# Optimization experiments

Hardware: AMD Instinct MI355X
Metric: run time of the kernel (lower is better)

The kernel has to match this reference:

```python
import jax, jax.numpy as jnp
import numpy as np

N_ATOMS, N_UND, N_DIR, N_ANG, N_STRUCT = 8192, 65536, 131072, 262144, 128
FEA, NRAD, NANGB, NCONV = 64, 9, 9, 4

FLOAT_NAMES = ["bond_bases_ag", "bond_bases_bg", "angle_bases", "atom_emb", "Wb", "Wa",
               "Wbw_ag", "Wbw_bg",
               "ac_cw1", "ac_cb1", "ac_cw2", "ac_cb2", "ac_gw1", "ac_gb1", "ac_gw2", "ac_gb2", "ac_out",
               "bc_cw1", "bc_cb1", "bc_cw2", "bc_cb2", "bc_gw1", "bc_gb1", "bc_gw2", "bc_gb2", "bc_out",
               "an_cw", "an_cb", "an_gw", "an_gb",
               "ro_w1", "ro_b1", "ro_w2", "ro_b2", "ro_w3", "ro_b3"]
INT_NAMES = ["atomic_numbers", "atom_graph", "directed2undirected",
             "bond_graph_atoms", "bond_graph_bonds", "atom_owners"]


def _silu(x):
    return x * jax.nn.sigmoid(x)


def _gmlp(x, cw1, cb1, cw2, cb2, gw1, gb1, gw2, gb2):
    # GatedMLP (norm=None): silu(MLP_core(x)) * sigmoid(MLP_gate(x)), each MLP = Lin-silu-Lin
    core = _silu(_silu(x @ cw1 + cb1) @ cw2 + cb2)
    gate = jax.nn.sigmoid(_silu(x @ gw1 + gb1) @ gw2 + gb2)
    return core * gate


def _forward(F, I):
    seg = jax.ops.segment_sum
    atom = F["atom_emb"][I["atomic_numbers"]]            # [N, 64]
    bond = F["bond_bases_ag"] @ F["Wb"]                  # [U, 64]
    angle = F["angle_bases"] @ F["Wa"]                   # [A, 64]
    bw_ag = F["bond_bases_ag"] @ F["Wbw_ag"]             # [U, 64]
    bw_bg = F["bond_bases_bg"] @ F["Wbw_bg"]             # [U, 64]
    ag0, ag1 = I["atom_graph"][:, 0], I["atom_graph"][:, 1]
    d2u = I["directed2undirected"]
    bgi, bgj = I["bond_graph_bonds"][:, 0], I["bond_graph_bonds"][:, 1]
    bga = I["bond_graph_atoms"]

    def atom_conv(i, atom, bond):
        msg = jnp.concatenate([atom[ag0], bond[d2u], atom[ag1]], axis=1)   # [E, 192]
        msg = _gmlp(msg, F["ac_cw1"][i], F["ac_cb1"][i], F["ac_cw2"][i], F["ac_cb2"][i],
                    F["ac_gw1"][i], F["ac_gb1"][i], F["ac_gw2"][i], F["ac_gb2"][i])
        msg = msg * bw_ag[d2u]
        # scatter-add to center atoms, linear mlp_out (no bias), resnet
        return atom + seg(msg, ag0, num_segments=N_ATOMS) @ F["ac_out"][i]

    for i in range(NCONV - 1):
        atom = atom_conv(i, atom, bond)
        # BondConv over bond graph (angles)
        tot = jnp.concatenate([bond[bgi], bond[bgj], angle, atom[bga]], axis=1)  # [A, 256]
        upd = _gmlp(tot, F["bc_cw1"][i], F["bc_cb1"][i], F["bc_cw2"][i], F["bc_cb2"][i],
                    F["bc_gw1"][i], F["bc_gb1"][i], F["bc_gw2"][i], F["bc_gb2"][i])
        upd = upd * bw_bg[bgi]
        bond = bond + seg(upd, bgi, num_segments=N_UND) @ F["bc_out"][i]
        # AngleUpdate (hidden_dim=0 -> single linear in each gated branch), resnet
        tot2 = jnp.concatenate([bond[bgi], bond[bgj], angle, atom[bga]], axis=1)
        angle = angle + _silu(tot2 @ F["an_cw"][i] + F["an_cb"][i]) * \
            jax.nn.sigmoid(tot2 @ F["an_gw"][i] + F["an_gb"][i])
    atom = atom_conv(NCONV - 1, atom, bond)

    # mlp_first readout: per-atom energy MLP then average pooling per structure
    e = _silu(atom @ F["ro_w1"] + F["ro_b1"])
    e = _silu(e @ F["ro_w2"] + F["ro_b2"])
    e = (e @ F["ro_w3"] + F["ro_b3"])[:, 0]              # [N]
    owners = I["atom_owners"]
    esum = seg(e, owners, num_segments=N_STRUCT)
    cnt = seg(jnp.ones_like(e), owners, num_segments=N_STRUCT)
    return esum / jnp.maximum(cnt, 1.0)                  # [N_STRUCT] energy/atom


def setup_inputs() -> dict:
    key = jax.random.key(0)
    ks = iter(jax.random.split(key, 64))

    def nrm(shape, fan_in):
        return jax.random.normal(next(ks), shape, dtype=jnp.float32) / np.float32(np.sqrt(fan_in))

    z = lambda *s: jnp.zeros(s, dtype=jnp.float32)
    inp = {}
    inp["atomic_numbers"] = jax.random.randint(next(ks), (N_ATOMS,), 0, 94, dtype=jnp.int32)
    inp["bond_bases_ag"] = jax.random.uniform(next(ks), (N_UND, NRAD), dtype=jnp.float32)
    inp["bond_bases_bg"] = jax.random.uniform(next(ks), (N_UND, NRAD), dtype=jnp.float32)
    inp["angle_bases"] = jax.random.uniform(next(ks), (N_ANG, NANGB), dtype=jnp.float32)
    inp["atom_graph"] = jax.random.randint(next(ks), (N_DIR, 2), 0, N_ATOMS, dtype=jnp.int32)
    inp["directed2undirected"] = jax.random.randint(next(ks), (N_DIR,), 0, N_UND, dtype=jnp.int32)
    inp["bond_graph_atoms"] = jax.random.randint(next(ks), (N_ANG,), 0, N_ATOMS, dtype=jnp.int32)
    inp["bond_graph_bonds"] = jax.random.randint(next(ks), (N_ANG, 2), 0, N_UND, dtype=jnp.int32)
    inp["atom_owners"] = jnp.sort(jax.random.randint(next(ks), (N_ATOMS,), 0, N_STRUCT, dtype=jnp.int32))
    inp["atom_emb"] = nrm((95, FEA), 1.0)
    inp["Wb"] = nrm((NRAD, FEA), NRAD)
    inp["Wa"] = nrm((NANGB, FEA), NANGB)
    inp["Wbw_ag"] = nrm((NRAD, FEA), NRAD)
    inp["Wbw_bg"] = nrm((NRAD, FEA), NRAD)
    d_a, d_b = 3 * FEA, 4 * FEA
    nb = NCONV - 1
    inp["ac_cw1"] = nrm((NCONV, d_a, FEA), d_a); inp["ac_cb1"] = z(NCONV, FEA)
    inp["ac_cw2"] = nrm((NCONV, FEA, FEA), FEA); inp["ac_cb2"] = z(NCONV, FEA)
    inp["ac_gw1"] = nrm((NCONV, d_a, FEA), d_a); inp["ac_gb1"] = z(NCONV, FEA)
    inp["ac_gw2"] = nrm((NCONV, FEA, FEA), FEA); inp["ac_gb2"] = z(NCONV, FEA)
    inp["ac_out"] = nrm((NCONV, FEA, FEA), FEA)
    inp["bc_cw1"] = nrm((nb, d_b, FEA), d_b); inp["bc_cb1"] = z(nb, FEA)
    inp["bc_cw2"] = nrm((nb, FEA, FEA), FEA); inp["bc_cb2"] = z(nb, FEA)
    inp["bc_gw1"] = nrm((nb, d_b, FEA), d_b); inp["bc_gb1"] = z(nb, FEA)
    inp["bc_gw2"] = nrm((nb, FEA, FEA), FEA); inp["bc_gb2"] = z(nb, FEA)
    inp["bc_out"] = nrm((nb, FEA, FEA), FEA)
    inp["an_cw"] = nrm((nb, d_b, FEA), d_b); inp["an_cb"] = z(nb, FEA)
    inp["an_gw"] = nrm((nb, d_b, FEA), d_b); inp["an_gb"] = z(nb, FEA)
    inp["ro_w1"] = nrm((FEA, FEA), FEA); inp["ro_b1"] = z(FEA)
    inp["ro_w2"] = nrm((FEA, FEA), FEA); inp["ro_b2"] = z(FEA)
    inp["ro_w3"] = nrm((FEA, 1), FEA); inp["ro_b3"] = z(1)
    return inp


def reference(atomic_numbers, bond_bases_ag, bond_bases_bg, angle_bases, atom_graph,
              directed2undirected, bond_graph_atoms, bond_graph_bonds, atom_owners,
              atom_emb, Wb, Wa, Wbw_ag, Wbw_bg,
              ac_cw1, ac_cb1, ac_cw2, ac_cb2, ac_gw1, ac_gb1, ac_gw2, ac_gb2, ac_out,
              bc_cw1, bc_cb1, bc_cw2, bc_cb2, bc_gw1, bc_gb1, bc_gw2, bc_gb2, bc_out,
              an_cw, an_cb, an_gw, an_gb,
              ro_w1, ro_b1, ro_w2, ro_b2, ro_w3, ro_b3):
    loc = locals()
    F = {k: loc[k] for k in FLOAT_NAMES}
    I = {k: loc[k] for k in INT_NAMES}
    return _forward(F, I)
```

## Files before the change

### kernel.cpp

```cpp
#include <hip/hip_runtime.h>
#include <hip/hip_bf16.h>

typedef float f32x4 __attribute__((ext_vector_type(4)));
typedef short s16x8 __attribute__((ext_vector_type(8)));
typedef unsigned int u32x4 __attribute__((ext_vector_type(4)));

#define DEV static __device__ __forceinline__

DEV unsigned short f2bf(float x){
    unsigned u = __builtin_bit_cast(unsigned, x);
    u += 0x7FFFu + ((u >> 16) & 1u);
    return (unsigned short)(u >> 16);
}
DEV float bf2f(unsigned short h){
    unsigned u = ((unsigned)h) << 16;
    return __builtin_bit_cast(float, u);
}
DEV float sigm_(float x){ return __builtin_amdgcn_rcpf(1.0f + __expf(-x)); }
DEV float silu_(float x){ return x * sigm_(x); }

__global__ __launch_bounds__(256) void k_transconv(const float* __restrict__ src,
                                                   unsigned short* __restrict__ dst,
                                                   int K, int total){
    int gid = blockIdx.x * 256 + threadIdx.x;
    if (gid >= total) return;
    int kn  = K * 64;
    int b   = gid / kn;
    int rem = gid - b * kn;
    int k   = rem >> 6, n = rem & 63;
    dst[b * kn + n * K + k] = f2bf(src[gid]);
}

__global__ __launch_bounds__(256) void k_embed(const float* __restrict__ emb,
                                               const int* __restrict__ z,
                                               unsigned short* __restrict__ out){
    int gid = blockIdx.x * 256 + threadIdx.x;
    int n = gid >> 6, f = gid & 63;
    out[gid] = f2bf(emb[z[n] * 64 + f]);
}

__global__ __launch_bounds__(256) void k_smallmm(const float* __restrict__ bases,
                                                 const float* __restrict__ W,
                                                 unsigned short* __restrict__ out){
    int gid = blockIdx.x * 256 + threadIdx.x;
    int r = gid >> 6, f = gid & 63;
    const float* b = bases + r * 9;
    float acc = 0.f;
    #pragma unroll
    for (int k = 0; k < 9; ++k) acc += b[k] * W[k * 64 + f];
    out[gid] = f2bf(acc);
}

__global__ void k_count(const int* __restrict__ dst, int stride, int n, int* __restrict__ cnt){
    int i = blockIdx.x * 256 + threadIdx.x;
    if (i < n) atomicAdd(&cnt[dst[(size_t)i * stride]], 1);
}

__global__ __launch_bounds__(256) void k_bsum(const int* __restrict__ cnt,
                                              int* __restrict__ bsum){
    int i = blockIdx.x * 256 + threadIdx.x;
    int v = cnt[i];
    #pragma unroll
    for (int off = 32; off > 0; off >>= 1) v += __shfl_down(v, off);
    __shared__ int ws[4];
    if ((threadIdx.x & 63) == 0) ws[threadIdx.x >> 6] = v;
    __syncthreads();
    if (threadIdx.x == 0) bsum[blockIdx.x] = ws[0] + ws[1] + ws[2] + ws[3];
}

__global__ __launch_bounds__(256) void k_bscan(const int* __restrict__ bsum,
                                               int* __restrict__ bbase, int nb,
                                               int* __restrict__ total_out){
    __shared__ int sh[256];
    int t = threadIdx.x;
    int v = (t < nb) ? bsum[t] : 0;
    sh[t] = v;
    __syncthreads();
    for (int d = 1; d < 256; d <<= 1){
        int u = (t >= d) ? sh[t - d] : 0;
        __syncthreads();
        sh[t] += u;
        __syncthreads();
    }
    if (t < nb) bbase[t] = sh[t] - v;
    if (t == nb - 1) *total_out = sh[t];
}

__global__ __launch_bounds__(256) void k_offs(const int* __restrict__ cnt,
                                              const int* __restrict__ bbase,
                                              int* __restrict__ offs){
    __shared__ int sh[256];
    int t = threadIdx.x;
    int i = blockIdx.x * 256 + t;
    int v = cnt[i];
    sh[t] = v;
    __syncthreads();
    for (int d = 1; d < 256; d <<= 1){
        int u = (t >= d) ? sh[t - d] : 0;
        __syncthreads();
        sh[t] += u;
        __syncthreads();
    }
    offs[i] = bbase[blockIdx.x] + sh[t] - v;
}

__global__ void k_fill(const int* __restrict__ dst, int stride, int n,
                       const int* __restrict__ offs, int* __restrict__ cur,
                       int* __restrict__ idx){
    int i = blockIdx.x * 256 + threadIdx.x;
    if (i < n){
        int d = dst[(size_t)i * stride];
        int p = offs[d] + atomicAdd(&cur[d], 1);
        idx[p] = i;
    }
}

__global__ __launch_bounds__(256) void k_reduce(const unsigned short* __restrict__ upd,
                                                const int* __restrict__ offs,
                                                const int* __restrict__ idx,
                                                unsigned short* __restrict__ act, int nRows){
    int gid = blockIdx.x * 256 + threadIdx.x;
    int row = gid >> 3;
    if (row >= nRows) return;
    int c8 = (gid & 7) * 8;
    int o = offs[row], e = offs[row + 1];
    float acc[8] = {};
    for (int j = o; j < e; ++j){
        s16x8 v = *(const s16x8*)&upd[(size_t)idx[j] * 64 + c8];
        #pragma unroll
        for (int q = 0; q < 8; ++q) acc[q] += bf2f((unsigned short)v[q]);
    }
    s16x8 a = *(s16x8*)&act[(size_t)row * 64 + c8];
    #pragma unroll
    for (int q = 0; q < 8; ++q) a[q] = (short)f2bf(bf2f((unsigned short)a[q]) + acc[q]);
    *(s16x8*)&act[(size_t)row * 64 + c8] = a;
}

#define MFMA16(a,b,c) __builtin_amdgcn_mfma_f32_16x16x32_bf16(a,b,c,0,0,0)

__global__ __launch_bounds__(256, 4) void k_atom_conv(
    const unsigned short* __restrict__ atomBf, const unsigned short* __restrict__ bondBf,
    const unsigned short* __restrict__ bwagBf,
    const int* __restrict__ agraph, const int* __restrict__ d2u,
    const unsigned short* __restrict__ w1cT, const unsigned short* __restrict__ w1gT,
    const unsigned short* __restrict__ w2cT, const unsigned short* __restrict__ w2gT,
    const unsigned short* __restrict__ woT,
    const float* __restrict__ cb1, const float* __restrict__ cb2,
    const float* __restrict__ gb1, const float* __restrict__ gb2,
    unsigned short* __restrict__ upd)
{
    __shared__ unsigned short lds[14208];
    __shared__ int ldsIdx[64];
    unsigned short* ldsA  = lds;
    unsigned short* ldsHC = lds;
    unsigned short* ldsHG = lds + 4736;
    unsigned short* ldsV  = lds + 9472;
    const int tid = threadIdx.x;
    const int r0  = blockIdx.x * 64;

    {
        const int srow = tid >> 2, q = tid & 3;
        int e = r0 + srow;
        if (q < 3){
            const unsigned short* src;
            if (q == 0)      src = atomBf + (size_t)agraph[2 * e] * 64;
            else if (q == 1){ int u = d2u[e]; ldsIdx[srow] = u; src = bondBf + (size_t)u * 64; }
            else             src = atomBf + (size_t)agraph[2 * e + 1] * 64;
            #pragma unroll
            for (int j = 0; j < 8; ++j)
                *(u32x4*)&ldsA[srow * 200 + q * 64 + j * 8] = *(const u32x4*)(src + j * 8);
        }
    }
    __syncthreads();

    const int lane = tid & 63;
    const int r16  = lane & 15;
    const int grp  = lane >> 4;
    const int col  = (tid >> 6) * 16 + r16;

    unsigned short bwv[16];
    #pragma unroll
    for (int mt = 0; mt < 4; ++mt)
        #pragma unroll
        for (int j = 0; j < 4; ++j)
            bwv[mt * 4 + j] = bwagBf[(size_t)ldsIdx[mt * 16 + grp * 4 + j] * 64 + col];

    f32x4 aC[4] = {}, aG[4] = {};
    #pragma unroll
    for (int kt = 0; kt < 6; ++kt){
        s16x8 bc = *(const s16x8*)&w1cT[col * 192 + kt * 32 + grp * 8];
        s16x8 bg = *(const s16x8*)&w1gT[col * 192 + kt * 32 + grp * 8];
        #pragma unroll
        for (int mt = 0; mt < 4; ++mt){
            s16x8 a = *(const s16x8*)&ldsA[(mt * 16 + r16) * 200 + kt * 32 + grp * 8];
            aC[mt] = MFMA16(a, bc, aC[mt]);
            aG[mt] = MFMA16(a, bg, aG[mt]);
        }
    }
    __syncthreads();

    const float bC1 = cb1[col], bG1 = gb1[col];
    #pragma unroll
    for (int mt = 0; mt < 4; ++mt){
        #pragma unroll
        for (int j = 0; j < 4; ++j){
            int row = mt * 16 + grp * 4 + j;
            ldsHC[row * 74 + col] = f2bf(silu_(aC[mt][j] + bC1));
            ldsHG[row * 74 + col] = f2bf(silu_(aG[mt][j] + bG1));
        }
    }
    __syncthreads();

    f32x4 oC[4] = {}, oG[4] = {};
    #pragma unroll
    for (int kt = 0; kt < 2; ++kt){
        s16x8 bc = *(const s16x8*)&w2cT[col * 64 + kt * 32 + grp * 8];
        s16x8 bg = *(const s16x8*)&w2gT[col * 64 + kt * 32 + grp * 8];
        #pragma unroll
        for (int mt = 0; mt < 4; ++mt){
            s16x8 hc = *(const s16x8*)&ldsHC[(mt * 16 + r16) * 74 + kt * 32 + grp * 8];
            s16x8 hg = *(const s16x8*)&ldsHG[(mt * 16 + r16) * 74 + kt * 32 + grp * 8];
            oC[mt] = MFMA16(hc, bc, oC[mt]);
            oG[mt] = MFMA16(hg, bg, oG[mt]);
        }
    }
    const float bC2 = cb2[col], bG2 = gb2[col];
    #pragma unroll
    for (int mt = 0; mt < 4; ++mt){
        #pragma unroll
        for (int j = 0; j < 4; ++j){
            int row = mt * 16 + grp * 4 + j;
            float v = silu_(oC[mt][j] + bC2) * sigm_(oG[mt][j] + bG2);
            v *= bf2f(bwv[mt * 4 + j]);
            ldsV[row * 74 + col] = f2bf(v);
        }
    }
    __syncthreads();

    f32x4 oD[4] = {};
    #pragma unroll
    for (int kt = 0; kt < 2; ++kt){
        s16x8 bo = *(const s16x8*)&woT[col * 64 + kt * 32 + grp * 8];
        #pragma unroll
        for (int mt = 0; mt < 4; ++mt){
            s16x8 a = *(const s16x8*)&ldsV[(mt * 16 + r16) * 74 + kt * 32 + grp * 8];
            oD[mt] = MFMA16(a, bo, oD[mt]);
        }
    }
    #pragma unroll
    for (int mt = 0; mt < 4; ++mt){
        #pragma unroll
        for (int j = 0; j < 4; ++j){
            int row = mt * 16 + grp * 4 + j;
            upd[(size_t)(r0 + row) * 64 + col] = f2bf(oD[mt][j]);
        }
    }
}

__global__ __launch_bounds__(256, 4) void k_bond_conv(
    const unsigned short* __restrict__ atomBf, const unsigned short* __restrict__ bondBf,
    const unsigned short* __restrict__ angleBf, const unsigned short* __restrict__ bwbgBf,
    const int* __restrict__ bga, const int* __restrict__ bgb,
    const unsigned short* __restrict__ w1cT, const unsigned short* __restrict__ w1gT,
    const unsigned short* __restrict__ w2cT, const unsigned short* __restrict__ w2gT,
    const unsigned short* __restrict__ woT,
    const float* __restrict__ cb1, const float* __restrict__ cb2,
    const float* __restrict__ gb1, const float* __restrict__ gb2,
    unsigned short* __restrict__ upd)
{
    __shared__ unsigned short lds[16896];
    __shared__ int ldsIdx[64];
    unsigned short* ldsA  = lds;
    unsigned short* ldsHC = lds;
    unsigned short* ldsHG = lds + 4736;
    unsigned short* ldsV  = lds + 9472;
    const int tid = threadIdx.x;
    const int r0  = blockIdx.x * 64;

    {
        const int srow = tid >> 2, q = tid & 3;
        int a = r0 + srow;
        const unsigned short* src;
        if (q == 0){ int2 bb = *(const int2*)&bgb[2 * a]; ldsIdx[srow] = bb.x;
                     src = bondBf + (size_t)bb.x * 64; }
        else if (q == 1){ src = bondBf  + (size_t)bgb[2 * a + 1] * 64; }
        else if (q == 2){ src = angleBf + (size_t)a * 64; }
        else            { src = atomBf  + (size_t)bga[a] * 64; }
        #pragma unroll
        for (int j = 0; j < 8; ++j)
            *(u32x4*)&ldsA[srow * 264 + q * 64 + j * 8] = *(const u32x4*)(src + j * 8);
    }
    __syncthreads();

    const int lane = tid & 63;
    const int r16  = lane & 15;
    const int grp  = lane >> 4;
    const int col  = (tid >> 6) * 16 + r16;

    unsigned short bwv[16];
    #pragma unroll
    for (int mt = 0; mt < 4; ++mt)
        #pragma unroll
        for (int j = 0; j < 4; ++j)
            bwv[mt * 4 + j] = bwbgBf[(size_t)ldsIdx[mt * 16 + grp * 4 + j] * 64 + col];

    f32x4 aC[4] = {}, aG[4] = {};
    #pragma unroll
    for (int kt = 0; kt < 8; ++kt){
        s16x8 bc = *(const s16x8*)&w1cT[col * 256 + kt * 32 + grp * 8];
        s16x8 bg = *(const s16x8*)&w1gT[col * 256 + kt * 32 + grp * 8];
        #pragma unroll
        for (int mt = 0; mt < 4; ++mt){
            s16x8 a = *(const s16x8*)&ldsA[(mt * 16 + r16) * 264 + kt * 32 + grp * 8];
            aC[mt] = MFMA16(a, bc, aC[mt]);
            aG[mt] = MFMA16(a, bg, aG[mt]);
        }
    }
    __syncthreads();

    const float bC1 = cb1[col], bG1 = gb1[col];
    #pragma unroll
    for (int mt = 0; mt < 4; ++mt){
        #pragma unroll
        for (int j = 0; j < 4; ++j){
            int row = mt * 16 + grp * 4 + j;
            ldsHC[row * 74 + col] = f2bf(silu_(aC[mt][j] + bC1));
            ldsHG[row * 74 + col] = f2bf(silu_(aG[mt][j] + bG1));
        }
    }
    __syncthreads();

    f32x4 oC[4] = {}, oG[4] = {};
    #pragma unroll
    for (int kt = 0; kt < 2; ++kt){
        s16x8 bc = *(const s16x8*)&w2cT[col * 64 + kt * 32 + grp * 8];
        s16x8 bg = *(const s16x8*)&w2gT[col * 64 + kt * 32 + grp * 8];
        #pragma unroll
        for (int mt = 0; mt < 4; ++mt){
            s16x8 hc = *(const s16x8*)&ldsHC[(mt * 16 + r16) * 74 + kt * 32 + grp * 8];
            s16x8 hg = *(const s16x8*)&ldsHG[(mt * 16 + r16) * 74 + kt * 32 + grp * 8];
            oC[mt] = MFMA16(hc, bc, oC[mt]);
            oG[mt] = MFMA16(hg, bg, oG[mt]);
        }
    }
    const float bC2 = cb2[col], bG2 = gb2[col];
    #pragma unroll
    for (int mt = 0; mt < 4; ++mt){
        #pragma unroll
        for (int j = 0; j < 4; ++j){
            int row = mt * 16 + grp * 4 + j;
            float v = silu_(oC[mt][j] + bC2) * sigm_(oG[mt][j] + bG2);
            v *= bf2f(bwv[mt * 4 + j]);
            ldsV[row * 74 + col] = f2bf(v);
        }
    }
    __syncthreads();

    f32x4 oD[4] = {};
    #pragma unroll
    for (int kt = 0; kt < 2; ++kt){
        s16x8 bo = *(const s16x8*)&woT[col * 64 + kt * 32 + grp * 8];
        #pragma unroll
        for (int mt = 0; mt < 4; ++mt){
            s16x8 a = *(const s16x8*)&ldsV[(mt * 16 + r16) * 74 + kt * 32 + grp * 8];
            oD[mt] = MFMA16(a, bo, oD[mt]);
        }
    }
    #pragma unroll
    for (int mt = 0; mt < 4; ++mt){
        #pragma unroll
        for (int j = 0; j < 4; ++j){
            int row = mt * 16 + grp * 4 + j;
            upd[(size_t)(r0 + row) * 64 + col] = f2bf(oD[mt][j]);
        }
    }
}

__global__ __launch_bounds__(256, 4) void k_angle(
    const unsigned short* __restrict__ atomBf, const unsigned short* __restrict__ bondBf,
    unsigned short* __restrict__ angleBf,
    const int* __restrict__ bga, const int* __restrict__ bgb,
    const unsigned short* __restrict__ wcT, const unsigned short* __restrict__ wgT,
    const float* __restrict__ cb, const float* __restrict__ gb)
{
    __shared__ unsigned short ldsA[64 * 264];
    const int tid = threadIdx.x;
    const int r0  = blockIdx.x * 64;

    {
        const int srow = tid >> 2, q = tid & 3;
        int a = r0 + srow;
        const unsigned short* src;
        if (q == 0)      src = bondBf  + (size_t)bgb[2 * a] * 64;
        else if (q == 1) src = bondBf  + (size_t)bgb[2 * a + 1] * 64;
        else if (q == 2) src = angleBf + (size_t)a * 64;
        else             src = atomBf  + (size_t)bga[a] * 64;
        #pragma unroll
        for (int j = 0; j < 8; ++j)
            *(u32x4*)&ldsA[srow * 264 + q * 64 + j * 8] = *(const u32x4*)(src + j * 8);
    }
    __syncthreads();

    const int lane = tid & 63;
    const int r16  = lane & 15;
    const int grp  = lane >> 4;
    const int col  = (tid >> 6) * 16 + r16;

    f32x4 aC[4] = {}, aG[4] = {};
    #pragma unroll
    for (int kt = 0; kt < 8; ++kt){
        s16x8 bc = *(const s16x8*)&wcT[col * 256 + kt * 32 + grp * 8];
        s16x8 bg = *(const s16x8*)&wgT[col * 256 + kt * 32 + grp * 8];
        #pragma unroll
        for (int mt = 0; mt < 4; ++mt){
            s16x8 a = *(const s16x8*)&ldsA[(mt * 16 + r16) * 264 + kt * 32 + grp * 8];
            aC[mt] = MFMA16(a, bc, aC[mt]);
            aG[mt] = MFMA16(a, bg, aG[mt]);
        }
    }
    const float bC = cb[col], bG = gb[col];
    #pragma unroll
    for (int mt = 0; mt < 4; ++mt){
        #pragma unroll
        for (int j = 0; j < 4; ++j){
            int row = mt * 16 + grp * 4 + j;
            int a = r0 + row;
            float oldv = bf2f(ldsA[row * 264 + 128 + col]);
            float v = silu_(aC[mt][j] + bC) * sigm_(aG[mt][j] + bG);
            angleBf[(size_t)a * 64 + col] = f2bf(oldv + v);
        }
    }
}

__global__ __launch_bounds__(256) void k_readout(
    const unsigned short* __restrict__ atomBf, const int* __restrict__ owners,
    const float* __restrict__ w1, const float* __restrict__ b1,
    const float* __restrict__ w2, const float* __restrict__ b2,
    const float* __restrict__ w3, const float* __restrict__ b3,
    float* __restrict__ esum, float* __restrict__ cnt)
{
    int gid  = blockIdx.x * 256 + threadIdx.x;
    int n    = gid >> 6;
    int lane = threadIdx.x & 63;
    float a = bf2f(atomBf[n * 64 + lane]);
    float acc = b1[lane];
    #pragma unroll
    for (int k = 0; k < 64; ++k) acc += __shfl(a, k) * w1[k * 64 + lane];
    float h = silu_(acc);
    acc = b2[lane];
    #pragma unroll
    for (int k = 0; k < 64; ++k) acc += __shfl(h, k) * w2[k * 64 + lane];
    h = silu_(acc);
    float p = h * w3[lane];
    #pragma unroll
    for (int off = 32; off > 0; off >>= 1) p += __shfl_xor(p, off);
    if (lane == 0){
        atomicAdd(&esum[owners[n]], p + b3[0]);
        atomicAdd(&cnt[owners[n]], 1.0f);
    }
}

__global__ void k_final(const float* __restrict__ esum, const float* __restrict__ cnt,
                        float* __restrict__ out){
    int i = threadIdx.x;
    if (i < 128) out[i] = esum[i] / fmaxf(cnt[i], 1.0f);
}

extern "C" void kernel_launch(void* const* d_in, const int* in_sizes, int n_in,
                              void* d_out, int out_size, void* d_ws, size_t ws_size,
                              hipStream_t stream)
{
    (void)in_sizes; (void)n_in; (void)out_size; (void)ws_size;
    const int N_ATOMS = 8192, N_UND = 65536, N_DIR = 131072, N_ANG = 262144;

    const int*   atomic_numbers = (const int*)  d_in[0];
    const float* bb_ag  = (const float*)d_in[1];
    const float* bb_bg  = (const float*)d_in[2];
    const float* ang_b  = (const float*)d_in[3];
    const int*   agraph = (const int*)  d_in[4];
    const int*   d2u    = (const int*)  d_in[5];
    const int*   bga    = (const int*)  d_in[6];
    const int*   bgb    = (const int*)  d_in[7];
    const int*   owners = (const int*)  d_in[8];
    const float* emb    = (const float*)d_in[9];
    const float* Wb     = (const float*)d_in[10];
    const float* Wa     = (const float*)d_in[11];
    const float* Wbwag  = (const float*)d_in[12];
    const float* Wbwbg  = (const float*)d_in[13];
    const float* ac_cw1 = (const float*)d_in[14];
    const float* ac_cb1 = (const float*)d_in[15];
    const float* ac_cw2 = (const float*)d_in[16];
    const float* ac_cb2 = (const float*)d_in[17];
    const float* ac_gw1 = (const float*)d_in[18];
    const float* ac_gb1 = (const float*)d_in[19];
    const float* ac_gw2 = (const float*)d_in[20];
    const float* ac_gb2 = (const float*)d_in[21];
    const float* ac_out = (const float*)d_in[22];
    const float* bc_cw1 = (const float*)d_in[23];
    const float* bc_cb1 = (const float*)d_in[24];
    const float* bc_cw2 = (const float*)d_in[25];
    const float* bc_cb2 = (const float*)d_in[26];
    const float* bc_gw1 = (const float*)d_in[27];
    const float* bc_gb1 = (const float*)d_in[28];
    const float* bc_gw2 = (const float*)d_in[29];
    const float* bc_gb2 = (const float*)d_in[30];
    const float* bc_out = (const float*)d_in[31];
    const float* an_cw  = (const float*)d_in[32];
    const float* an_cb  = (const float*)d_in[33];
    const float* an_gw  = (const float*)d_in[34];
    const float* an_gb  = (const float*)d_in[35];
    const float* ro_w1  = (const float*)d_in[36];
    const float* ro_b1  = (const float*)d_in[37];
    const float* ro_w2  = (const float*)d_in[38];
    const float* ro_b2  = (const float*)d_in[39];
    const float* ro_w3  = (const float*)d_in[40];
    const float* ro_b3  = (const float*)d_in[41];

    char* ws = (char*)d_ws;
    size_t off = 0;
    auto alloc = [&](size_t bytes) -> void* {
        void* p = ws + off;
        off = (off + bytes + 255) & ~(size_t)255;
        return p;
    };
    unsigned short* atomBf  = (unsigned short*)alloc((size_t)N_ATOMS * 64 * 2);
    unsigned short* bondBf  = (unsigned short*)alloc((size_t)N_UND   * 64 * 2);
    unsigned short* angleBf = (unsigned short*)alloc((size_t)N_ANG   * 64 * 2);
    unsigned short* bwagBf  = (unsigned short*)alloc((size_t)N_UND   * 64 * 2);
    unsigned short* bwbgBf  = (unsigned short*)alloc((size_t)N_UND   * 64 * 2);
    unsigned short* updBuf  = (unsigned short*)alloc((size_t)N_ANG   * 64 * 2);
    float* esum   = (float*)alloc(128 * 4);
    float* cnt    = (float*)alloc(128 * 4);
    int* offsA = (int*)alloc((N_ATOMS + 1) * 4);
    int* curA  = (int*)alloc(N_ATOMS * 4);
    int* idxA  = (int*)alloc((size_t)N_DIR * 4);
    int* offsB = (int*)alloc((N_UND + 1) * 4);
    int* curB  = (int*)alloc(N_UND * 4);
    int* idxB  = (int*)alloc((size_t)N_ANG * 4);
    int* bsum  = (int*)alloc(256 * 4);
    int* bbase = (int*)alloc(256 * 4);
    unsigned short* acw1cT = (unsigned short*)alloc((size_t)4 * 64 * 192 * 2);
    unsigned short* acw1gT = (unsigned short*)alloc((size_t)4 * 64 * 192 * 2);
    unsigned short* acw2cT = (unsigned short*)alloc((size_t)4 * 64 * 64 * 2);
    unsigned short* acw2gT = (unsigned short*)alloc((size_t)4 * 64 * 64 * 2);
    unsigned short* acoT   = (unsigned short*)alloc((size_t)4 * 64 * 64 * 2);
    unsigned short* bcw1cT = (unsigned short*)alloc((size_t)3 * 64 * 256 * 2);
    unsigned short* bcw1gT = (unsigned short*)alloc((size_t)3 * 64 * 256 * 2);
    unsigned short* bcw2cT = (unsigned short*)alloc((size_t)3 * 64 * 64 * 2);
    unsigned short* bcw2gT = (unsigned short*)alloc((size_t)3 * 64 * 64 * 2);
    unsigned short* bcoT   = (unsigned short*)alloc((size_t)3 * 64 * 64 * 2);
    unsigned short* anwcT  = (unsigned short*)alloc((size_t)3 * 64 * 256 * 2);
    unsigned short* anwgT  = (unsigned short*)alloc((size_t)3 * 64 * 256 * 2);

    auto tc = [&](const float* src, unsigned short* dst, int B, int K){
        int total = B * K * 64;
        k_transconv<<<(total + 255) / 256, 256, 0, stream>>>(src, dst, K, total);
    };
    tc(ac_cw1, acw1cT, 4, 192);  tc(ac_gw1, acw1gT, 4, 192);
    tc(ac_cw2, acw2cT, 4, 64);   tc(ac_gw2, acw2gT, 4, 64);
    tc(ac_out, acoT,   4, 64);
    tc(bc_cw1, bcw1cT, 3, 256);  tc(bc_gw1, bcw1gT, 3, 256);
    tc(bc_cw2, bcw2cT, 3, 64);   tc(bc_gw2, bcw2gT, 3, 64);
    tc(bc_out, bcoT,   3, 64);
    tc(an_cw,  anwcT,  3, 256);  tc(an_gw,  anwgT,  3, 256);

    k_embed<<<N_ATOMS * 64 / 256, 256, 0, stream>>>(emb, atomic_numbers, atomBf);
    k_smallmm<<<N_UND * 64 / 256, 256, 0, stream>>>(bb_ag, Wb,    bondBf);
    k_smallmm<<<N_ANG * 64 / 256, 256, 0, stream>>>(ang_b, Wa,    angleBf);
    k_smallmm<<<N_UND * 64 / 256, 256, 0, stream>>>(bb_ag, Wbwag, bwagBf);
    k_smallmm<<<N_UND * 64 / 256, 256, 0, stream>>>(bb_bg, Wbwbg, bwbgBf);

    hipMemsetAsync(curA, 0, N_ATOMS * 4, stream);
    k_count<<<(N_DIR + 255) / 256, 256, 0, stream>>>(agraph, 2, N_DIR, curA);
    k_bsum <<<N_ATOMS / 256, 256, 0, stream>>>(curA, bsum);
    k_bscan<<<1, 256, 0, stream>>>(bsum, bbase, N_ATOMS / 256, offsA + N_ATOMS);
    k_offs <<<N_ATOMS / 256, 256, 0, stream>>>(curA, bbase, offsA);
    hipMemsetAsync(curA, 0, N_ATOMS * 4, stream);
    k_fill<<<(N_DIR + 255) / 256, 256, 0, stream>>>(agraph, 2, N_DIR, offsA, curA, idxA);

    hipMemsetAsync(curB, 0, N_UND * 4, stream);
    k_count<<<(N_ANG + 255) / 256, 256, 0, stream>>>(bgb, 2, N_ANG, curB);
    k_bsum <<<N_UND / 256, 256, 0, stream>>>(curB, bsum);
    k_bscan<<<1, 256, 0, stream>>>(bsum, bbase, N_UND / 256, offsB + N_UND);
    k_offs <<<N_UND / 256, 256, 0, stream>>>(curB, bbase, offsB);
    hipMemsetAsync(curB, 0, N_UND * 4, stream);
    k_fill<<<(N_ANG + 255) / 256, 256, 0, stream>>>(bgb, 2, N_ANG, offsB, curB, idxB);

    for (int i = 0; i < 4; ++i){
        k_atom_conv<<<N_DIR / 64, 256, 0, stream>>>(
            atomBf, bondBf, bwagBf, agraph, d2u,
            acw1cT + (size_t)i * 64 * 192, acw1gT + (size_t)i * 64 * 192,
            acw2cT + (size_t)i * 64 * 64,  acw2gT + (size_t)i * 64 * 64,
            acoT   + (size_t)i * 64 * 64,
            ac_cb1 + i * 64, ac_cb2 + i * 64, ac_gb1 + i * 64, ac_gb2 + i * 64, updBuf);
        k_reduce<<<N_ATOMS * 8 / 256, 256, 0, stream>>>(updBuf, offsA, idxA, atomBf, N_ATOMS);
        if (i == 3) break;
        k_bond_conv<<<N_ANG / 64, 256, 0, stream>>>(
            atomBf, bondBf, angleBf, bwbgBf, bga, bgb,
            bcw1cT + (size_t)i * 64 * 256, bcw1gT + (size_t)i * 64 * 256,
            bcw2cT + (size_t)i * 64 * 64,  bcw2gT + (size_t)i * 64 * 64,
            bcoT   + (size_t)i * 64 * 64,
            bc_cb1 + i * 64, bc_cb2 + i * 64, bc_gb1 + i * 64, bc_gb2 + i * 64, updBuf);
        k_reduce<<<N_UND * 8 / 256, 256, 0, stream>>>(updBuf, offsB, idxB, bondBf, N_UND);
        k_angle<<<N_ANG / 64, 256, 0, stream>>>(
            atomBf, bondBf, angleBf, bga, bgb,
            anwcT + (size_t)i * 64 * 256, anwgT + (size_t)i * 64 * 256,
            an_cb + i * 64, an_gb + i * 64);
    }

    hipMemsetAsync(esum, 0, 128 * 4, stream);
    hipMemsetAsync(cnt,  0, 128 * 4, stream);
    k_readout<<<N_ATOMS * 64 / 256, 256, 0, stream>>>(
        atomBf, owners, ro_w1, ro_b1, ro_w2, ro_b2, ro_w3, ro_b3, esum, cnt);
    k_final<<<1, 128, 0, stream>>>(esum, cnt, (float*)d_out);
}
```

Before: 913.2 us.

## Process edges in destination-sorted order so segment reduce reads contiguous rows

The atom, bond and angle conv kernels now visit edges and angles through the CSR permutation (idxA/idxB). They write each update row at its sorted position, so k_reduce sums a contiguous range instead of gathering rows through idx. The gather phase is rebuilt as two stages: first resolve source indices into LDS, then issue cooperative 16-byte row loads. The atom conv also stages the bw_ag rows in LDS instead of doing scattered per-element loads. This trades the reduce's indirect reads for one extra indirection in the conv kernels, plus angle writes that are now scattered.

```diff
diff --git a/kernel.cpp b/kernel.cpp
--- a/kernel.cpp
+++ b/kernel.cpp
@@ -117,7 +117,6 @@
 
 __global__ __launch_bounds__(256) void k_reduce(const unsigned short* __restrict__ upd,
                                                 const int* __restrict__ offs,
-                                                const int* __restrict__ idx,
                                                 unsigned short* __restrict__ act, int nRows){
     int gid = blockIdx.x * 256 + threadIdx.x;
     int row = gid >> 3;
@@ -126,7 +125,7 @@
     int o = offs[row], e = offs[row + 1];
     float acc[8] = {};
     for (int j = o; j < e; ++j){
-        s16x8 v = *(const s16x8*)&upd[(size_t)idx[j] * 64 + c8];
+        s16x8 v = *(const s16x8*)&upd[(size_t)j * 64 + c8];
         #pragma unroll
         for (int q = 0; q < 8; ++q) acc[q] += bf2f((unsigned short)v[q]);
     }
@@ -142,6 +141,7 @@
     const unsigned short* __restrict__ atomBf, const unsigned short* __restrict__ bondBf,
     const unsigned short* __restrict__ bwagBf,
     const int* __restrict__ agraph, const int* __restrict__ d2u,
+    const int* __restrict__ idxA,
     const unsigned short* __restrict__ w1cT, const unsigned short* __restrict__ w1gT,
     const unsigned short* __restrict__ w2cT, const unsigned short* __restrict__ w2gT,
     const unsigned short* __restrict__ woT,
@@ -150,7 +150,8 @@
     unsigned short* __restrict__ upd)
 {
     __shared__ unsigned short lds[14208];
-    __shared__ int ldsIdx[64];
+    __shared__ unsigned short ldsBw[64 * 68];
+    __shared__ int ldsSrc[256];
     unsigned short* ldsA  = lds;
     unsigned short* ldsHC = lds;
     unsigned short* ldsHG = lds + 4736;
@@ -159,16 +160,28 @@
     const int r0  = blockIdx.x * 64;
 
     {
-        const int srow = tid >> 2, q = tid & 3;
-        int e = r0 + srow;
-        if (q < 3){
-            const unsigned short* src;
-            if (q == 0)      src = atomBf + (size_t)agraph[2 * e] * 64;
-            else if (q == 1){ int u = d2u[e]; ldsIdx[srow] = u; src = bondBf + (size_t)u * 64; }
-            else             src = atomBf + (size_t)agraph[2 * e + 1] * 64;
-            #pragma unroll
-            for (int j = 0; j < 8; ++j)
-                *(u32x4*)&ldsA[srow * 200 + q * 64 + j * 8] = *(const u32x4*)(src + j * 8);
+        int q = tid >> 6, row = tid & 63;
+        int e = idxA[r0 + row];
+        int s;
+        if (q == 0)      s = agraph[2 * e];
+        else if (q == 1) s = d2u[e];
+        else if (q == 2) s = agraph[2 * e + 1];
+        else             s = d2u[e];
+        ldsSrc[tid] = s;
+    }
+    __syncthreads();
+    {
+        const int lane8 = tid & 7;
+        #pragma unroll
+        for (int p = 0; p < 8; ++p){
+            int cc = p * 32 + (tid >> 3);
+            int q = cc >> 6, row = cc & 63;
+            int s = ldsSrc[cc];
+            const unsigned short* buf = (q == 1 || q == 3) ? bondBf : atomBf;
+            if (q == 3) buf = bwagBf;
+            u32x4 v = *(const u32x4*)(buf + (size_t)s * 64 + lane8 * 8);
+            if (q < 3) *(u32x4*)&ldsA[row * 200 + q * 64 + lane8 * 8] = v;
+            else       *(u32x4*)&ldsBw[row * 68 + lane8 * 8] = v;
         }
     }
     __syncthreads();
@@ -177,13 +190,6 @@
     const int r16  = lane & 15;
     const int grp  = lane >> 4;
     const int col  = (tid >> 6) * 16 + r16;
-
-    unsigned short bwv[16];
-    #pragma unroll
-    for (int mt = 0; mt < 4; ++mt)
-        #pragma unroll
-        for (int j = 0; j < 4; ++j)
-            bwv[mt * 4 + j] = bwagBf[(size_t)ldsIdx[mt * 16 + grp * 4 + j] * 64 + col];
 
     f32x4 aC[4] = {}, aG[4] = {};
     #pragma unroll
@@ -231,7 +237,7 @@
         for (int j = 0; j < 4; ++j){
             int row = mt * 16 + grp * 4 + j;
             float v = silu_(oC[mt][j] + bC2) * sigm_(oG[mt][j] + bG2);
-            v *= bf2f(bwv[mt * 4 + j]);
+            v *= bf2f(ldsBw[row * 68 + col]);
             ldsV[row * 74 + col] = f2bf(v);
         }
     }
@@ -261,6 +267,7 @@
     const unsigned short* __restrict__ atomBf, const unsigned short* __restrict__ bondBf,
     const unsigned short* __restrict__ angleBf, const unsigned short* __restrict__ bwbgBf,
     const int* __restrict__ bga, const int* __restrict__ bgb,
+    const int* __restrict__ idxB,
     const unsigned short* __restrict__ w1cT, const unsigned short* __restrict__ w1gT,
     const unsigned short* __restrict__ w2cT, const unsigned short* __restrict__ w2gT,
     const unsigned short* __restrict__ woT,
@@ -269,7 +276,7 @@
     unsigned short* __restrict__ upd)
 {
     __shared__ unsigned short lds[16896];
-    __shared__ int ldsIdx[64];
+    __shared__ int ldsSrc[256];
     unsigned short* ldsA  = lds;
     unsigned short* ldsHC = lds;
     unsigned short* ldsHG = lds + 4736;
@@ -278,17 +285,27 @@
     const int r0  = blockIdx.x * 64;
 
     {
-        const int srow = tid >> 2, q = tid & 3;
-        int a = r0 + srow;
-        const unsigned short* src;
-        if (q == 0){ int2 bb = *(const int2*)&bgb[2 * a]; ldsIdx[srow] = bb.x;
-                     src = bondBf + (size_t)bb.x * 64; }
-        else if (q == 1){ src = bondBf  + (size_t)bgb[2 * a + 1] * 64; }
-        else if (q == 2){ src = angleBf + (size_t)a * 64; }
-        else            { src = atomBf  + (size_t)bga[a] * 64; }
-        #pragma unroll
-        for (int j = 0; j < 8; ++j)
-            *(u32x4*)&ldsA[srow * 264 + q * 64 + j * 8] = *(const u32x4*)(src + j * 8);
+        int q = tid >> 6, row = tid & 63;
+        int a = idxB[r0 + row];
+        int s;
+        if (q == 0)      s = bgb[2 * a];
+        else if (q == 1) s = bgb[2 * a + 1];
+        else if (q == 2) s = a;
+        else             s = bga[a];
+        ldsSrc[tid] = s;
+    }
+    __syncthreads();
+    {
+        const int lane8 = tid & 7;
+        #pragma unroll
+        for (int p = 0; p < 8; ++p){
+            int cc = p * 32 + (tid >> 3);
+            int q = cc >> 6, row = cc & 63;
+            int s = ldsSrc[cc];
+            const unsigned short* buf = (q < 2) ? bondBf : (q == 2 ? angleBf : atomBf);
+            u32x4 v = *(const u32x4*)(buf + (size_t)s * 64 + lane8 * 8);
+            *(u32x4*)&ldsA[row * 264 + q * 64 + lane8 * 8] = v;
+        }
     }
     __syncthreads();
 
@@ -302,7 +319,7 @@
     for (int mt = 0; mt < 4; ++mt)
         #pragma unroll
         for (int j = 0; j < 4; ++j)
-            bwv[mt * 4 + j] = bwbgBf[(size_t)ldsIdx[mt * 16 + grp * 4 + j] * 64 + col];
+            bwv[mt * 4 + j] = bwbgBf[(size_t)ldsSrc[mt * 16 + grp * 4 + j] * 64 + col];
 
     f32x4 aC[4] = {}, aG[4] = {};
     #pragma unroll
@@ -380,24 +397,37 @@
     const unsigned short* __restrict__ atomBf, const unsigned short* __restrict__ bondBf,
     unsigned short* __restrict__ angleBf,
     const int* __restrict__ bga, const int* __restrict__ bgb,
+    const int* __restrict__ idxB,
     const unsigned short* __restrict__ wcT, const unsigned short* __restrict__ wgT,
     const float* __restrict__ cb, const float* __restrict__ gb)
 {
     __shared__ unsigned short ldsA[64 * 264];
+    __shared__ int ldsSrc[256];
     const int tid = threadIdx.x;
     const int r0  = blockIdx.x * 64;
 
     {
-        const int srow = tid >> 2, q = tid & 3;
-        int a = r0 + srow;
-        const unsigned short* src;
-        if (q == 0)      src = bondBf  + (size_t)bgb[2 * a] * 64;
-        else if (q == 1) src = bondBf  + (size_t)bgb[2 * a + 1] * 64;
-        else if (q == 2) src = angleBf + (size_t)a * 64;
-        else             src = atomBf  + (size_t)bga[a] * 64;
-        #pragma unroll
-        for (int j = 0; j < 8; ++j)
-            *(u32x4*)&ldsA[srow * 264 + q * 64 + j * 8] = *(const u32x4*)(src + j * 8);
+        int q = tid >> 6, row = tid & 63;
+        int a = idxB[r0 + row];
+        int s;
+        if (q == 0)      s = bgb[2 * a];
+        else if (q == 1) s = bgb[2 * a + 1];
+        else if (q == 2) s = a;
+        else             s = bga[a];
+        ldsSrc[tid] = s;
+    }
+    __syncthreads();
+    {
+        const int lane8 = tid & 7;
+        #pragma unroll
+        for (int p = 0; p < 8; ++p){
+            int cc = p * 32 + (tid >> 3);
+            int q = cc >> 6, row = cc & 63;
+            int s = ldsSrc[cc];
+            const unsigned short* buf = (q < 2) ? bondBf : (q == 2 ? angleBf : atomBf);
+            u32x4 v = *(const u32x4*)(buf + (size_t)s * 64 + lane8 * 8);
+            *(u32x4*)&ldsA[row * 264 + q * 64 + lane8 * 8] = v;
+        }
     }
     __syncthreads();
 
@@ -424,7 +454,7 @@
         #pragma unroll
         for (int j = 0; j < 4; ++j){
             int row = mt * 16 + grp * 4 + j;
-            int a = r0 + row;
+            int a = ldsSrc[128 + row];
             float oldv = bf2f(ldsA[row * 264 + 128 + col]);
             float v = silu_(aC[mt][j] + bC) * sigm_(aG[mt][j] + bG);
             angleBf[(size_t)a * 64 + col] = f2bf(oldv + v);
@@ -588,22 +618,22 @@
 
     for (int i = 0; i < 4; ++i){
         k_atom_conv<<<N_DIR / 64, 256, 0, stream>>>(
-            atomBf, bondBf, bwagBf, agraph, d2u,
+            atomBf, bondBf, bwagBf, agraph, d2u, idxA,
             acw1cT + (size_t)i * 64 * 192, acw1gT + (size_t)i * 64 * 192,
             acw2cT + (size_t)i * 64 * 64,  acw2gT + (size_t)i * 64 * 64,
             acoT   + (size_t)i * 64 * 64,
             ac_cb1 + i * 64, ac_cb2 + i * 64, ac_gb1 + i * 64, ac_gb2 + i * 64, updBuf);
-        k_reduce<<<N_ATOMS * 8 / 256, 256, 0, stream>>>(updBuf, offsA, idxA, atomBf, N_ATOMS);
+        k_reduce<<<N_ATOMS * 8 / 256, 256, 0, stream>>>(updBuf, offsA, atomBf, N_ATOMS);
         if (i == 3) break;
         k_bond_conv<<<N_ANG / 64, 256, 0, stream>>>(
-            atomBf, bondBf, angleBf, bwbgBf, bga, bgb,
+            atomBf, bondBf, angleBf, bwbgBf, bga, bgb, idxB,
             bcw1cT + (size_t)i * 64 * 256, bcw1gT + (size_t)i * 64 * 256,
             bcw2cT + (size_t)i * 64 * 64,  bcw2gT + (size_t)i * 64 * 64,
             bcoT   + (size_t)i * 64 * 64,
             bc_cb1 + i * 64, bc_cb2 + i * 64, bc_gb1 + i * 64, bc_gb2 + i * 64, updBuf);
-        k_reduce<<<N_UND * 8 / 256, 256, 0, stream>>>(updBuf, offsB, idxB, bondBf, N_UND);
+        k_reduce<<<N_UND * 8 / 256, 256, 0, stream>>>(updBuf, offsB, bondBf, N_UND);
         k_angle<<<N_ANG / 64, 256, 0, stream>>>(
-            atomBf, bondBf, angleBf, bga, bgb,
+            atomBf, bondBf, angleBf, bga, bgb, idxB,
             anwcT + (size_t)i * 64 * 256, anwgT + (size_t)i * 64 * 256,
             an_cb + i * 64, an_gb + i * 64);
     }
```

Result: faster. 874.0 us (-4.3%).
